# Optimization experiments

Measured on AMD Instinct MI355X. Metric: run time of the kernel, lower is better.

## Reference

```python
import jax, jax.numpy as jnp
import numpy as np

H = 96
NH = 4
HD = H // NH
SPARSITY = 0.5
LN_EPS = 1e-5


def _lstm_layer(xs, w_ih, w_hh, b_ih, b_hh):
    # xs: [B, T, I]; PyTorch gate order i, f, g, o
    B = xs.shape[0]
    Hd = w_hh.shape[1]
    def step(carry, x_t):
        h, c = carry
        gates = x_t @ w_ih.T + h @ w_hh.T + b_ih + b_hh  # [B, 4H]
        i, f, g, o = jnp.split(gates, 4, axis=-1)
        i = jax.nn.sigmoid(i); f = jax.nn.sigmoid(f)
        g = jnp.tanh(g); o = jax.nn.sigmoid(o)
        c = f * c + i * g
        h = o * jnp.tanh(c)
        return (h, c), h
    h0 = jnp.zeros((B, Hd), xs.dtype)
    c0 = jnp.zeros((B, Hd), xs.dtype)
    _, hs = jax.lax.scan(step, (h0, c0), xs.transpose(1, 0, 2))  # [T, B, H]
    return hs.transpose(1, 0, 2)


def _layer_norm(x, w, b):
    mu = jnp.mean(x, axis=-1, keepdims=True)
    var = jnp.mean((x - mu) ** 2, axis=-1, keepdims=True)
    return (x - mu) * jax.lax.rsqrt(var + LN_EPS) * w + b


def _split_heads(x, B, T):
    return x.reshape(B, T, NH, HD).transpose(0, 2, 1, 3)  # [B, H, T, d]


def _sparse_attention(x, qw, kw, vw, ow):
    B, T, _ = x.shape
    q = _split_heads(x @ qw.T, B, T)
    k = _split_heads(x @ kw.T, B, T)
    v = _split_heads(x @ vw.T, B, T)
    scores = jnp.einsum('bhtd,bhsd->bhts', q, k) / np.sqrt(HD).astype(np.float32)
    num_keep = int(T * SPARSITY)
    topv, _ = jax.lax.top_k(scores, num_keep)
    kth = topv[..., -1:]  # threshold == k-th largest (equiv to topk+scatter mask for distinct values)
    scores = jnp.where(scores >= kth, scores, -jnp.inf)
    attn = jax.nn.softmax(scores, axis=-1)  # dropout is identity in eval
    out = jnp.einsum('bhts,bhsd->bhtd', attn, v)
    out = out.transpose(0, 2, 1, 3).reshape(B, T, H)
    return out @ ow.T


def _mha(x, in_w, in_b, out_w, out_b):
    B, T, _ = x.shape
    qkv = x @ in_w.T + in_b  # [B, T, 3H]
    q, k, v = jnp.split(qkv, 3, axis=-1)
    q = _split_heads(q, B, T); k = _split_heads(k, B, T); v = _split_heads(v, B, T)
    scores = jnp.einsum('bhtd,bhsd->bhts', q, k) / np.sqrt(HD).astype(np.float32)
    attn = jax.nn.softmax(scores, axis=-1)
    out = jnp.einsum('bhts,bhsd->bhtd', attn, v)
    out = out.transpose(0, 2, 1, 3).reshape(B, T, H)
    return out @ out_w.T + out_b


def _encoder_layer(x, in_w, in_b, out_w, out_b, l1_w, l1_b, l2_w, l2_b, ln1_w, ln1_b, ln2_w, ln2_b):
    # PyTorch TransformerEncoderLayer, post-norm, ReLU, eval (no dropout)
    x = _layer_norm(x + _mha(x, in_w, in_b, out_w, out_b), ln1_w, ln1_b)
    ff = jax.nn.relu(x @ l1_w.T + l1_b) @ l2_w.T + l2_b
    return _layer_norm(x + ff, ln2_w, ln2_b)


def setup_inputs() -> dict:
    key = jax.random.key(0)
    ks = iter(jax.random.split(key, 40))
    B, T, I = 16, 1024, 64
    FF = 2 * H
    def rnd(shape, scale=0.05):
        return (jax.random.normal(next(ks), shape, dtype=jnp.float32) * scale)
    inp = {
        'x': jax.random.normal(next(ks), (B, T, I), dtype=jnp.float32),
        'w_ih0': rnd((4 * H, I)), 'w_hh0': rnd((4 * H, H)),
        'b_ih0': rnd((4 * H,)), 'b_hh0': rnd((4 * H,)),
        'w_ih1': rnd((4 * H, H)), 'w_hh1': rnd((4 * H, H)),
        'b_ih1': rnd((4 * H,)), 'b_hh1': rnd((4 * H,)),
        'qw': rnd((H, H)), 'kw': rnd((H, H)), 'vw': rnd((H, H)), 'ow': rnd((H, H)),
        'enc_in_w': rnd((2, 3 * H, H)), 'enc_in_b': rnd((2, 3 * H)),
        'enc_out_w': rnd((2, H, H)), 'enc_out_b': rnd((2, H)),
        'enc_l1_w': rnd((2, FF, H)), 'enc_l1_b': rnd((2, FF)),
        'enc_l2_w': rnd((2, H, FF)), 'enc_l2_b': rnd((2, H)),
        'enc_ln1_w': jnp.ones((2, H), jnp.float32), 'enc_ln1_b': jnp.zeros((2, H), jnp.float32),
        'enc_ln2_w': jnp.ones((2, H), jnp.float32), 'enc_ln2_b': jnp.zeros((2, H), jnp.float32),
        'fc_w': rnd((1, H)), 'fc_b': rnd((1,)),
    }
    return inp


def reference(x, w_ih0, w_hh0, b_ih0, b_hh0, w_ih1, w_hh1, b_ih1, b_hh1,
              qw, kw, vw, ow,
              enc_in_w, enc_in_b, enc_out_w, enc_out_b,
              enc_l1_w, enc_l1_b, enc_l2_w, enc_l2_b,
              enc_ln1_w, enc_ln1_b, enc_ln2_w, enc_ln2_b,
              fc_w, fc_b):
    h = _lstm_layer(x, w_ih0, w_hh0, b_ih0, b_hh0)
    h = _lstm_layer(h, w_ih1, w_hh1, b_ih1, b_hh1)
    h = _sparse_attention(h, qw, kw, vw, ow)
    for i in range(2):
        h = _encoder_layer(h, enc_in_w[i], enc_in_b[i], enc_out_w[i], enc_out_b[i],
                           enc_l1_w[i], enc_l1_b[i], enc_l2_w[i], enc_l2_b[i],
                           enc_ln1_w[i], enc_ln1_b[i], enc_ln2_w[i], enc_ln2_b[i])
    return h[:, -1, :] @ fc_w.T + fc_b  # [B, 1]
```

## Files before the change

kernel.cpp:

```cpp
#include <hip/hip_runtime.h>
#include <cstdint>
#include <cmath>

#define T_SEQ 1024
#define BATCH 16
#define HID 96
#define G4 384
#define QKV_LD 288
#define HDIM 24
#define KKEEP 512
#define SCALE 0.20412414523193154f

__device__ __forceinline__ float wred_sum(float v){
#pragma unroll
  for (int o=32;o;o>>=1) v += __shfl_xor(v,o,64);
  return v;
}
__device__ __forceinline__ float wred_max(float v){
#pragma unroll
  for (int o=32;o;o>>=1) v = fmaxf(v,__shfl_xor(v,o,64));
  return v;
}
__device__ __forceinline__ int wred_sumi(int v){
#pragma unroll
  for (int o=32;o;o>>=1) v += __shfl_xor(v,o,64);
  return v;
}
__device__ __forceinline__ unsigned fmono(float f){
  unsigned u = __float_as_uint(f);
  return (u & 0x80000000u) ? ~u : (u | 0x80000000u);
}
__device__ __forceinline__ float fast_sig(float x){
  return __builtin_amdgcn_rcpf(1.f + __expf(-x));
}
__device__ __forceinline__ float fast_tanh(float x){
  return 1.f - 2.f*__builtin_amdgcn_rcpf(1.f + __expf(2.f*x));
}

__global__ __launch_bounds__(256)
void gemm_kernel(const float* __restrict__ A, const float* __restrict__ W,
                 const float* __restrict__ b1, const float* __restrict__ b2,
                 float* __restrict__ C, int M, int N, int K,
                 int ldc, int coff, int relu)
{
  __shared__ float As[16][68];
  __shared__ float Ws[16][68];
  const int tid = threadIdx.x;
  const int tx = tid & 15, ty = tid >> 4;
  const int m0 = blockIdx.y * 64, n0 = blockIdx.x * 64;
  const int lrow = tid >> 2, lcol = (tid & 3) * 4;
  float acc[4][4] = {};
  for (int k0 = 0; k0 < K; k0 += 16) {
    float4 a = {0,0,0,0}, w = {0,0,0,0};
    int gm = m0 + lrow;
    if (gm < M) a = *(const float4*)(A + (size_t)gm*K + k0 + lcol);
    int gn = n0 + lrow;
    if (gn < N) w = *(const float4*)(W + (size_t)gn*K + k0 + lcol);
    __syncthreads();
    As[lcol+0][lrow]=a.x; As[lcol+1][lrow]=a.y; As[lcol+2][lrow]=a.z; As[lcol+3][lrow]=a.w;
    Ws[lcol+0][lrow]=w.x; Ws[lcol+1][lrow]=w.y; Ws[lcol+2][lrow]=w.z; Ws[lcol+3][lrow]=w.w;
    __syncthreads();
#pragma unroll
    for (int kk=0;kk<16;++kk){
      const float4 av = *(const float4*)&As[kk][ty*4];
      const float4 wv = *(const float4*)&Ws[kk][tx*4];
      float a_[4]={av.x,av.y,av.z,av.w};
      float w_[4]={wv.x,wv.y,wv.z,wv.w};
#pragma unroll
      for (int i=0;i<4;++i)
#pragma unroll
        for (int j=0;j<4;++j) acc[i][j] += a_[i]*w_[j];
    }
  }
#pragma unroll
  for (int i=0;i<4;++i){
    int gm = m0 + ty*4 + i;
    if (gm >= M) continue;
#pragma unroll
    for (int j=0;j<4;++j){
      int gn = n0 + tx*4 + j;
      if (gn >= N) continue;
      float v = acc[i][j];
      if (b1) v += b1[gn];
      if (b2) v += b2[gn];
      if (relu) v = fmaxf(v, 0.f);
      C[(size_t)gm*ldc + coff + gn] = v;
    }
  }
}

__global__ __launch_bounds__(768)
void lstm_kernel(const float* __restrict__ pre, const float* __restrict__ w_hh,
                 float* __restrict__ hout)
{
  const int b = blockIdx.x;
  const int tid = threadIdx.x;
  const int g = tid >> 1, half = tid & 1;
  float w[48];
  {
    const float* wp = w_hh + g*96 + half*48;
#pragma unroll
    for (int j=0;j<48;j+=4){
      float4 t = *(const float4*)(wp + j);
      w[j]=t.x; w[j+1]=t.y; w[j+2]=t.z; w[j+3]=t.w;
    }
  }
  __shared__ float h_lds[96];
  __shared__ float gate_lds[384];
  float c = 0.f;
  if (tid < 96) h_lds[tid] = 0.f;
  __syncthreads();
  const float* prow = pre + (size_t)b*T_SEQ*G4 + g;
  float* hrow = hout + (size_t)b*T_SEQ*HID;
  float pf[4];
#pragma unroll
  for (int i=0;i<4;++i) pf[i] = prow[(size_t)i*G4];
  for (int tb=0; tb<T_SEQ; tb+=4){
#pragma unroll
    for (int u=0; u<4; ++u){
      const int t = tb + u;
      const float pcur = pf[u];
      int tn = t + 4; if (tn > T_SEQ-1) tn = T_SEQ-1;
      pf[u] = prow[(size_t)tn*G4];
      const float* hb = h_lds + half*48;
      float a0=0.f,a1=0.f,a2=0.f,a3=0.f;
#pragma unroll
      for (int j=0;j<48;j+=4){
        a0 += w[j]*hb[j]; a1 += w[j+1]*hb[j+1];
        a2 += w[j+2]*hb[j+2]; a3 += w[j+3]*hb[j+3];
      }
      float acc = (a0+a1)+(a2+a3);
      acc += __shfl_xor(acc, 1, 64);
      if (half == 0) gate_lds[g] = acc + pcur;
      __syncthreads();
      if (tid < 96){
        float ig = gate_lds[tid], fg = gate_lds[96+tid];
        float gg = gate_lds[192+tid], og = gate_lds[288+tid];
        float is = fast_sig(ig);
        float fs = fast_sig(fg);
        float gt = fast_tanh(gg);
        float os = fast_sig(og);
        c = fs*c + is*gt;
        float hv = os * fast_tanh(c);
        h_lds[tid] = hv;
        hrow[t*HID + tid] = hv;
      }
      __syncthreads();
    }
  }
}

__global__ __launch_bounds__(512)
void attn_kernel(const float* __restrict__ qkv, float* __restrict__ out, int sparse)
{
  __shared__ float kl[24][260];
  const int tid = threadIdx.x;
  const int wave = tid >> 6, lane = tid & 63;
  const int bh = blockIdx.x >> 7;
  const int b = bh >> 2, h = bh & 3;
  const int tq = ((blockIdx.x & 127) << 3) + wave;
  const size_t base = (size_t)b * T_SEQ;
  const int hoff = h * HDIM;
  float q[24];
  {
    const float* qp = qkv + (base + tq)*QKV_LD + hoff;
#pragma unroll
    for (int d4=0; d4<6; ++d4){
      float4 t = *(const float4*)(qp + d4*4);
      q[d4*4]=t.x; q[d4*4+1]=t.y; q[d4*4+2]=t.z; q[d4*4+3]=t.w;
    }
  }
  float sc[16];
  for (int c=0;c<4;++c){
    __syncthreads();
#pragma unroll
    for (int rep=0;rep<3;++rep){
      int p = rep*512 + tid;
      int sl = p/6, d4 = p - sl*6;
      const float4 kv = *(const float4*)(qkv + (base + (c<<8) + sl)*QKV_LD + 96 + hoff + d4*4);
      kl[d4*4+0][sl]=kv.x; kl[d4*4+1][sl]=kv.y; kl[d4*4+2][sl]=kv.z; kl[d4*4+3][sl]=kv.w;
    }
    __syncthreads();
    float a0=0.f,a1=0.f,a2=0.f,a3=0.f;
#pragma unroll
    for (int d=0; d<24; ++d){
      const float4 kd = *(const float4*)&kl[d][lane*4];
      a0 += q[d]*kd.x; a1 += q[d]*kd.y; a2 += q[d]*kd.z; a3 += q[d]*kd.w;
    }
    sc[c*4+0]=a0*SCALE; sc[c*4+1]=a1*SCALE; sc[c*4+2]=a2*SCALE; sc[c*4+3]=a3*SCALE;
  }
  float m_loc = sc[0];
#pragma unroll
  for (int i=1;i<16;++i) m_loc = fmaxf(m_loc, sc[i]);
  const float m = wred_max(m_loc);
  float sum_loc = 0.f;
  if (sparse){
    unsigned u[16];
#pragma unroll
    for (int i=0;i<16;++i) u[i] = fmono(sc[i]);
    unsigned prefix = 0;
    for (int bit=31; bit>=0; --bit){
      unsigned test = prefix | (1u<<bit);
      int cnt = 0;
#pragma unroll
      for (int i=0;i<16;++i) cnt += (u[i] >= test) ? 1 : 0;
      cnt = wred_sumi(cnt);
      if (cnt >= KKEEP) prefix = test;
    }
#pragma unroll
    for (int i=0;i<16;++i){
      float e = (u[i] >= prefix) ? __expf(sc[i]-m) : 0.f;
      sc[i] = e; sum_loc += e;
    }
  } else {
#pragma unroll
    for (int i=0;i<16;++i){
      float e = __expf(sc[i]-m);
      sc[i] = e; sum_loc += e;
    }
  }
  const float inv = 1.f / wred_sum(sum_loc);
#pragma unroll
  for (int i=0;i<16;++i) sc[i] *= inv;
  float acc[24] = {};
  for (int c=0;c<4;++c){
    __syncthreads();
#pragma unroll
    for (int rep=0;rep<3;++rep){
      int p = rep*512 + tid;
      int sl = p/6, d4 = p - sl*6;
      const float4 vv = *(const float4*)(qkv + (base + (c<<8) + sl)*QKV_LD + 192 + hoff + d4*4);
      kl[d4*4+0][sl]=vv.x; kl[d4*4+1][sl]=vv.y; kl[d4*4+2][sl]=vv.z; kl[d4*4+3][sl]=vv.w;
    }
    __syncthreads();
    const float w0=sc[c*4], w1=sc[c*4+1], w2=sc[c*4+2], w3=sc[c*4+3];
#pragma unroll
    for (int d=0; d<24; ++d){
      const float4 vd = *(const float4*)&kl[d][lane*4];
      acc[d] += w0*vd.x + w1*vd.y + w2*vd.z + w3*vd.w;
    }
  }
#pragma unroll
  for (int d=0; d<24; ++d) acc[d] = wred_sum(acc[d]);
  if (lane == 0){
    float* op = out + (base + tq)*HID + hoff;
#pragma unroll
    for (int d4=0; d4<6; ++d4){
      float4 t = {acc[d4*4], acc[d4*4+1], acc[d4*4+2], acc[d4*4+3]};
      *(float4*)(op + d4*4) = t;
    }
  }
}

__global__ __launch_bounds__(64)
void attn_last_kernel(const float* __restrict__ qkv, float* __restrict__ out)
{
  const int bh = blockIdx.x, b = bh>>2, h = bh&3;
  const int lane = threadIdx.x;
  const size_t base = (size_t)b*T_SEQ;
  const int hoff = h*HDIM;
  float q[24];
  {
    const float* qp = qkv + (base + T_SEQ-1)*QKV_LD + hoff;
#pragma unroll
    for (int d4=0; d4<6; ++d4){
      float4 t = *(const float4*)(qp + d4*4);
      q[d4*4]=t.x; q[d4*4+1]=t.y; q[d4*4+2]=t.z; q[d4*4+3]=t.w;
    }
  }
  float sc[16];
#pragma unroll 4
  for (int i=0;i<16;++i){
    const float* kp = qkv + (base + i*64 + lane)*QKV_LD + 96 + hoff;
    float a = 0.f;
#pragma unroll
    for (int d4=0; d4<6; ++d4){
      float4 kv = *(const float4*)(kp + d4*4);
      a += q[d4*4]*kv.x + q[d4*4+1]*kv.y + q[d4*4+2]*kv.z + q[d4*4+3]*kv.w;
    }
    sc[i] = a*SCALE;
  }
  float m_loc = sc[0];
#pragma unroll
  for (int i=1;i<16;++i) m_loc = fmaxf(m_loc, sc[i]);
  const float m = wred_max(m_loc);
  float sum_loc = 0.f;
#pragma unroll
  for (int i=0;i<16;++i){ sc[i] = __expf(sc[i]-m); sum_loc += sc[i]; }
  const float inv = 1.f / wred_sum(sum_loc);
  float acc[24] = {};
#pragma unroll 4
  for (int i=0;i<16;++i){
    const float* vp = qkv + (base + i*64 + lane)*QKV_LD + 192 + hoff;
    const float wgt = sc[i]*inv;
#pragma unroll
    for (int d4=0; d4<6; ++d4){
      float4 vv = *(const float4*)(vp + d4*4);
      acc[d4*4]   += wgt*vv.x; acc[d4*4+1] += wgt*vv.y;
      acc[d4*4+2] += wgt*vv.z; acc[d4*4+3] += wgt*vv.w;
    }
  }
#pragma unroll
  for (int d=0; d<24; ++d) acc[d] = wred_sum(acc[d]);
  if (lane == 0){
    float* op = out + (base + T_SEQ-1)*HID + hoff;
#pragma unroll
    for (int d4=0; d4<6; ++d4){
      float4 t = {acc[d4*4], acc[d4*4+1], acc[d4*4+2], acc[d4*4+3]};
      *(float4*)(op + d4*4) = t;
    }
  }
}

__global__ __launch_bounds__(256)
void resln_kernel(const float* __restrict__ x, const float* __restrict__ y,
                  const float* __restrict__ w, const float* __restrict__ bb,
                  float* __restrict__ out)
{
  const int row = blockIdx.x*4 + (threadIdx.x>>6);
  const int lane = threadIdx.x & 63;
  const float* xr = x + (size_t)row*HID;
  const float* yr = y + (size_t)row*HID;
  float v0 = xr[lane] + yr[lane];
  float v1 = (lane < 32) ? (xr[64+lane] + yr[64+lane]) : 0.f;
  float mu = wred_sum(v0+v1) * (1.f/96.f);
  float d0 = v0-mu, d1 = (lane<32) ? (v1-mu) : 0.f;
  float var = wred_sum(d0*d0 + d1*d1) * (1.f/96.f);
  float rs = rsqrtf(var + 1e-5f);
  float* orow = out + (size_t)row*HID;
  orow[lane] = d0*rs*w[lane] + bb[lane];
  if (lane < 32) orow[64+lane] = d1*rs*w[64+lane] + bb[64+lane];
}

__device__ __forceinline__ float block_sum_192(float v, float* red){
  v = wred_sum(v);
  const int tid = threadIdx.x;
  if ((tid & 63) == 0) red[tid>>6] = v;
  __syncthreads();
  float r = red[0]+red[1]+red[2];
  __syncthreads();
  return r;
}

__global__ __launch_bounds__(192)
void tail_kernel(const float* __restrict__ xin, const float* __restrict__ mha,
                 const float* __restrict__ out_w, const float* __restrict__ out_b,
                 const float* __restrict__ l1_w, const float* __restrict__ l1_b,
                 const float* __restrict__ l2_w, const float* __restrict__ l2_b,
                 const float* __restrict__ ln1w, const float* __restrict__ ln1b,
                 const float* __restrict__ ln2w, const float* __restrict__ ln2b,
                 const float* __restrict__ fcw, const float* __restrict__ fcb,
                 float* __restrict__ outp)
{
  const int b = blockIdx.x, tid = threadIdx.x;
  __shared__ float y[96], f1[192], mrow[96], red[3];
  const size_t row = ((size_t)b*T_SEQ + T_SEQ-1)*HID;
  if (tid < 96) mrow[tid] = mha[row + tid];
  __syncthreads();
  float r = 0.f;
  if (tid < 96){
    float p = out_b[tid];
    const float* wr = out_w + tid*96;
#pragma unroll 4
    for (int d=0; d<96; ++d) p += mrow[d]*wr[d];
    r = xin[row + tid] + p;
  }
  float mu = block_sum_192(tid<96 ? r : 0.f, red) * (1.f/96.f);
  float dv = tid<96 ? r-mu : 0.f;
  float var = block_sum_192(dv*dv, red) * (1.f/96.f);
  float rs = rsqrtf(var + 1e-5f);
  if (tid < 96) y[tid] = dv*rs*ln1w[tid] + ln1b[tid];
  __syncthreads();
  {
    float a = l1_b[tid];
    const float* wr = l1_w + tid*96;
#pragma unroll 4
    for (int d=0; d<96; ++d) a += y[d]*wr[d];
    f1[tid] = fmaxf(a, 0.f);
  }
  __syncthreads();
  float r2 = 0.f;
  if (tid < 96){
    float a = l2_b[tid];
    const float* wr = l2_w + tid*192;
#pragma unroll 4
    for (int d=0; d<192; ++d) a += f1[d]*wr[d];
    r2 = y[tid] + a;
  }
  float mu2 = block_sum_192(tid<96 ? r2 : 0.f, red) * (1.f/96.f);
  float dv2 = tid<96 ? r2-mu2 : 0.f;
  float var2 = block_sum_192(dv2*dv2, red) * (1.f/96.f);
  float rs2 = rsqrtf(var2 + 1e-5f);
  float z = tid<96 ? (dv2*rs2*ln2w[tid] + ln2b[tid]) : 0.f;
  float tot = block_sum_192(tid<96 ? z*fcw[tid] : 0.f, red);
  if (tid == 0) outp[b] = tot + fcb[0];
}

extern "C" void kernel_launch(void* const* d_in, const int* in_sizes, int n_in,
                              void* d_out, int out_size, void* d_ws, size_t ws_size,
                              hipStream_t stream)
{
  const float* x     = (const float*)d_in[0];
  const float* w_ih0 = (const float*)d_in[1];
  const float* w_hh0 = (const float*)d_in[2];
  const float* b_ih0 = (const float*)d_in[3];
  const float* b_hh0 = (const float*)d_in[4];
  const float* w_ih1 = (const float*)d_in[5];
  const float* w_hh1 = (const float*)d_in[6];
  const float* b_ih1 = (const float*)d_in[7];
  const float* b_hh1 = (const float*)d_in[8];
  const float* qw = (const float*)d_in[9];
  const float* kw = (const float*)d_in[10];
  const float* vw = (const float*)d_in[11];
  const float* ow = (const float*)d_in[12];
  const float* enc_in_w  = (const float*)d_in[13];
  const float* enc_in_b  = (const float*)d_in[14];
  const float* enc_out_w = (const float*)d_in[15];
  const float* enc_out_b = (const float*)d_in[16];
  const float* enc_l1_w  = (const float*)d_in[17];
  const float* enc_l1_b  = (const float*)d_in[18];
  const float* enc_l2_w  = (const float*)d_in[19];
  const float* enc_l2_b  = (const float*)d_in[20];
  const float* enc_ln1_w = (const float*)d_in[21];
  const float* enc_ln1_b = (const float*)d_in[22];
  const float* enc_ln2_w = (const float*)d_in[23];
  const float* enc_ln2_b = (const float*)d_in[24];
  const float* fc_w = (const float*)d_in[25];
  const float* fc_b = (const float*)d_in[26];
  float* outp = (float*)d_out;

  float* ws = (float*)d_ws;
  const size_t MT = (size_t)BATCH*T_SEQ;
  float* pre  = ws;
  float* bufA = pre  + MT*G4;
  float* bufB = bufA + MT*HID;
  float* bufC = bufB + MT*HID;

  const int M = (int)MT;
  auto gemm = [&](const float* A, const float* W, const float* bb1, const float* bb2,
                  float* C, int N, int K, int ldc, int coff, int relu){
    dim3 grid((N+63)/64, M/64);
    gemm_kernel<<<grid, dim3(256), 0, stream>>>(A, W, bb1, bb2, C, M, N, K, ldc, coff, relu);
  };

  gemm(x, w_ih0, b_ih0, b_hh0, pre, 384, 64, 384, 0, 0);
  lstm_kernel<<<dim3(BATCH), dim3(768), 0, stream>>>(pre, w_hh0, bufA);
  gemm(bufA, w_ih1, b_ih1, b_hh1, pre, 384, 96, 384, 0, 0);
  lstm_kernel<<<dim3(BATCH), dim3(768), 0, stream>>>(pre, w_hh1, bufB);
  gemm(bufB, qw, nullptr, nullptr, pre, 96, 96, QKV_LD, 0,   0);
  gemm(bufB, kw, nullptr, nullptr, pre, 96, 96, QKV_LD, 96,  0);
  gemm(bufB, vw, nullptr, nullptr, pre, 96, 96, QKV_LD, 192, 0);
  attn_kernel<<<dim3(8192), dim3(512), 0, stream>>>(pre, bufA, 1);
  gemm(bufA, ow, nullptr, nullptr, bufB, 96, 96, 96, 0, 0);
  gemm(bufB, enc_in_w, enc_in_b, nullptr, pre, 288, 96, QKV_LD, 0, 0);
  attn_kernel<<<dim3(8192), dim3(512), 0, stream>>>(pre, bufA, 0);
  gemm(bufA, enc_out_w, enc_out_b, nullptr, bufC, 96, 96, 96, 0, 0);
  resln_kernel<<<dim3(4096), dim3(256), 0, stream>>>(bufB, bufC, enc_ln1_w, enc_ln1_b, bufB);
  gemm(bufB, enc_l1_w, enc_l1_b, nullptr, pre, 192, 96, 192, 0, 1);
  gemm(pre, enc_l2_w, enc_l2_b, nullptr, bufC, 96, 192, 96, 0, 0);
  resln_kernel<<<dim3(4096), dim3(256), 0, stream>>>(bufB, bufC, enc_ln2_w, enc_ln2_b, bufB);
  gemm(bufB, enc_in_w + 288*96, enc_in_b + 288, nullptr, pre, 288, 96, QKV_LD, 0, 0);
  attn_last_kernel<<<dim3(64), dim3(64), 0, stream>>>(pre, bufA);
  tail_kernel<<<dim3(BATCH), dim3(192), 0, stream>>>(
      bufB, bufA,
      enc_out_w + 96*96, enc_out_b + 96,
      enc_l1_w + 192*96, enc_l1_b + 192,
      enc_l2_w + 96*192, enc_l2_b + 96,
      enc_ln1_w + 96, enc_ln1_b + 96,
      enc_ln2_w + 96, enc_ln2_b + 96,
      fc_w, fc_b, outp);
}
```

Before: 2.259 ms.

## Remap LSTM gate threads so each hidden unit's four gates share a wave

Reassigns threads in the LSTM recurrence so the eight lanes for one hidden unit (four gates, two halves each) sit together in a wave. The gate values are exchanged with lane shuffles instead of a shared-memory gate buffer, which removes one block barrier per timestep. Each lane applies its own activation through a uniform sigmoid/tanh formula built on exp2, and the cell update is computed redundantly across the eight lanes. This adds shuffles and redundant math per step in return for the saved barrier and LDS round trip.

```diff
diff --git a/kernel.cpp b/kernel.cpp
--- a/kernel.cpp
+++ b/kernel.cpp
@@ -10,6 +10,7 @@
 #define HDIM 24
 #define KKEEP 512
 #define SCALE 0.20412414523193154f
+#define L2E 1.4426950408889634f
 
 __device__ __forceinline__ float wred_sum(float v){
 #pragma unroll
@@ -29,12 +30,6 @@
 __device__ __forceinline__ unsigned fmono(float f){
   unsigned u = __float_as_uint(f);
   return (u & 0x80000000u) ? ~u : (u | 0x80000000u);
-}
-__device__ __forceinline__ float fast_sig(float x){
-  return __builtin_amdgcn_rcpf(1.f + __expf(-x));
-}
-__device__ __forceinline__ float fast_tanh(float x){
-  return 1.f - 2.f*__builtin_amdgcn_rcpf(1.f + __expf(2.f*x));
 }
 
 __global__ __launch_bounds__(256)
@@ -95,26 +90,33 @@
 {
   const int b = blockIdx.x;
   const int tid = threadIdx.x;
-  const int g = tid >> 1, half = tid & 1;
+  const int half = tid & 1, gid = (tid >> 1) & 3, j = tid >> 3;
+  const int grow = gid * 96 + j;
   float w[48];
   {
-    const float* wp = w_hh + g*96 + half*48;
-#pragma unroll
-    for (int j=0;j<48;j+=4){
-      float4 t = *(const float4*)(wp + j);
-      w[j]=t.x; w[j+1]=t.y; w[j+2]=t.z; w[j+3]=t.w;
-    }
-  }
+    const float* wp = w_hh + grow*96 + half*48;
+#pragma unroll
+    for (int k=0;k<48;k+=4){
+      float4 t = *(const float4*)(wp + k);
+      w[k]=t.x; w[k+1]=t.y; w[k+2]=t.z; w[k+3]=t.w;
+    }
+  }
+  const float Ac = (gid==2) ? 1.f : 0.f;
+  const float Bc = (gid==2) ? -2.f : 1.f;
+  const float Cc = (gid==2) ? 2.f*L2E : -L2E;
+  const bool g0 = (gid==0), g1 = (gid==1), g2 = (gid==2), g3 = (gid==3);
+
   __shared__ float h_lds[96];
-  __shared__ float gate_lds[384];
   float c = 0.f;
   if (tid < 96) h_lds[tid] = 0.f;
   __syncthreads();
-  const float* prow = pre + (size_t)b*T_SEQ*G4 + g;
+
+  const float* prow = pre + (size_t)b*T_SEQ*G4 + grow;
   float* hrow = hout + (size_t)b*T_SEQ*HID;
   float pf[4];
 #pragma unroll
   for (int i=0;i<4;++i) pf[i] = prow[(size_t)i*G4];
+
   for (int tb=0; tb<T_SEQ; tb+=4){
 #pragma unroll
     for (int u=0; u<4; ++u){
@@ -125,25 +127,26 @@
       const float* hb = h_lds + half*48;
       float a0=0.f,a1=0.f,a2=0.f,a3=0.f;
 #pragma unroll
-      for (int j=0;j<48;j+=4){
-        a0 += w[j]*hb[j]; a1 += w[j+1]*hb[j+1];
-        a2 += w[j+2]*hb[j+2]; a3 += w[j+3]*hb[j+3];
+      for (int k=0;k<48;k+=4){
+        a0 += w[k]*hb[k];   a1 += w[k+1]*hb[k+1];
+        a2 += w[k+2]*hb[k+2]; a3 += w[k+3]*hb[k+3];
       }
       float acc = (a0+a1)+(a2+a3);
-      acc += __shfl_xor(acc, 1, 64);
-      if (half == 0) gate_lds[g] = acc + pcur;
-      __syncthreads();
-      if (tid < 96){
-        float ig = gate_lds[tid], fg = gate_lds[96+tid];
-        float gg = gate_lds[192+tid], og = gate_lds[288+tid];
-        float is = fast_sig(ig);
-        float fs = fast_sig(fg);
-        float gt = fast_tanh(gg);
-        float os = fast_sig(og);
-        c = fs*c + is*gt;
-        float hv = os * fast_tanh(c);
-        h_lds[tid] = hv;
-        hrow[t*HID + tid] = hv;
+      const float full = acc + __shfl_xor(acc, 1, 64) + pcur;
+      const float act = fmaf(Bc, __builtin_amdgcn_rcpf(1.f + __builtin_amdgcn_exp2f(Cc*full)), Ac);
+      const float x1 = __shfl_xor(act, 2, 64);
+      const float x2 = __shfl_xor(act, 4, 64);
+      const float x3 = __shfl_xor(act, 6, 64);
+      const float iv = g0?act : g1?x1 : g2?x2 : x3;
+      const float fv = g1?act : g0?x1 : g3?x2 : x3;
+      const float gv = g2?act : g3?x1 : g0?x2 : x3;
+      const float ov = g3?act : g2?x1 : g1?x2 : x3;
+      c = fmaf(fv, c, iv*gv);
+      const float th = fmaf(-2.f, __builtin_amdgcn_rcpf(1.f + __builtin_amdgcn_exp2f(c*(2.f*L2E))), 1.f);
+      const float hv = ov*th;
+      if ((tid & 7) == 0){
+        h_lds[j] = hv;
+        hrow[t*HID + j] = hv;
       }
       __syncthreads();
     }
```

After: 2.222 ms. Within noise of the previous version (-1.7%).
